# Performance work log

Hardware: AMD Instinct MI355X
Metric: run time of the kernel (lower is better)

Reference implementation:

```python
import jax, jax.numpy as jnp
import numpy as np

NP_, NT_, D_, E_, EP_, L_, R_ = 100000, 300000, 64, 2000000, 500000, 2, 2


def setup_inputs() -> dict:
    key = jax.random.key(0)
    ks = jax.random.split(key, 12)
    return {
        "emb_playlist": jax.random.normal(ks[0], (NP_, D_), jnp.float32),
        "emb_track": jax.random.normal(ks[1], (NT_, D_), jnp.float32),
        "W_rel": jax.random.normal(ks[2], (L_, R_, D_, D_), jnp.float32) * 0.1,
        "W_root": jax.random.normal(ks[3], (L_, D_, D_), jnp.float32) * 0.1,
        "bias": jnp.zeros((L_, D_), jnp.float32),
        "n_id_playlist": jnp.arange(NP_, dtype=jnp.int32),
        "n_id_track": jnp.arange(NT_, dtype=jnp.int32),
        "edge_pt_src": jax.random.randint(ks[4], (E_,), 0, NP_, jnp.int32),
        "edge_pt_dst": jax.random.randint(ks[5], (E_,), 0, NT_, jnp.int32),
        "edge_tp_src": jax.random.randint(ks[6], (E_,), 0, NT_, jnp.int32),
        "edge_tp_dst": jax.random.randint(ks[7], (E_,), 0, NP_, jnp.int32),
        "ell_pl": jax.random.randint(ks[8], (EP_,), 0, NP_, jnp.int32),
        "ell_tr": jax.random.randint(ks[9], (EP_,), 0, NT_, jnp.int32),
    }


def _hetero_gnn(emb_playlist, emb_track, W_rel, W_root, bias,
                n_id_playlist, n_id_track,
                edge_pt_src, edge_pt_dst, edge_tp_src, edge_tp_dst,
                ell_pl, ell_tr):
    NP = emb_playlist.shape[0]
    NT = emb_track.shape[0]
    L = W_root.shape[0]
    N = NP + NT

    # embedding lookup by n_id (identity here, but faithful gather)
    x_pl = emb_playlist[n_id_playlist]
    x_tr = emb_track[n_id_track]

    # alpha=None -> uniform 1/(L+1); buffer is softmaxed -> still uniform
    weights = jax.nn.softmax(jnp.full((L + 1,), 1.0 / (L + 1), jnp.float32))

    out_pl = x_pl * weights[0]
    out_tr = x_tr * weights[0]

    # homogeneous layout: playlists at [0, NP), tracks at [NP, NP+NT)
    x = jnp.concatenate([x_pl, x_tr], axis=0)
    rel_edges = [
        (edge_pt_src, edge_pt_dst + NP),   # playlist -> track
        (edge_tp_src + NP, edge_tp_dst),   # track -> playlist
    ]

    for i in range(L):
        # RGCNConv: root transform + per-relation mean aggregation
        h = x @ W_root[i] + bias[i]
        for r, (src, dst) in enumerate(rel_edges):
            hr = x @ W_rel[i, r]              # [N, D] transform-then-gather
            msg = hr[src]                     # [E, D]
            ssum = jax.ops.segment_sum(msg, dst, num_segments=N)
            cnt = jax.ops.segment_sum(jnp.ones_like(dst, dtype=x.dtype), dst,
                                      num_segments=N)
            h = h + ssum / jnp.maximum(cnt, 1.0)[:, None]
        x = jax.nn.relu(h)
        out_pl = out_pl + x[:NP] * weights[i + 1]
        out_tr = out_tr + x[NP:] * weights[i + 1]

    # global -> local mapping via searchsorted (faithful happy path)
    ps_idx = jnp.argsort(n_id_playlist)
    ps = n_id_playlist[ps_idx]
    pl_loc = ps_idx[jnp.clip(jnp.searchsorted(ps, ell_pl), 0, NP - 1)]
    ts_idx = jnp.argsort(n_id_track)
    ts = n_id_track[ts_idx]
    tr_loc = ts_idx[jnp.clip(jnp.searchsorted(ts, ell_tr), 0, NT - 1)]

    # dot-product link scores (dropout p=0.0 -> identity)
    return jnp.sum(out_pl[pl_loc] * out_tr[tr_loc], axis=-1)


def reference(emb_playlist, emb_track, W_rel, W_root, bias,
              n_id_playlist, n_id_track,
              edge_pt_src, edge_pt_dst, edge_tp_src, edge_tp_dst,
              ell_pl, ell_tr):
    return _hetero_gnn(emb_playlist, emb_track, W_rel, W_root, bias,
                       n_id_playlist, n_id_track,
                       edge_pt_src, edge_pt_dst, edge_tp_src, edge_tp_dst,
                       ell_pl, ell_tr)
```

## Files before the change

kernel.cpp:

```cpp
#include <hip/hip_runtime.h>
#include <stdint.h>

typedef __attribute__((ext_vector_type(8))) short bf16x8;
typedef __attribute__((ext_vector_type(4))) float f32x4;

#define BN 192

static __device__ __forceinline__ float b2f_lo(uint32_t w) {
  union { uint32_t u; float f; } c; c.u = w << 16; return c.f;
}
static __device__ __forceinline__ float b2f_hi(uint32_t w) {
  union { uint32_t u; float f; } c; c.u = w & 0xffff0000u; return c.f;
}
static __device__ __forceinline__ uint16_t f2b(float f) {
  union { float f; uint32_t u; } c; c.f = f;
  return (uint16_t)((c.u + 0x7fffu + ((c.u >> 16) & 1u)) >> 16);
}
static __device__ __forceinline__ f32x4 unpack4(uint2 t) {
  f32x4 r;
  r.x = b2f_lo(t.x); r.y = b2f_hi(t.x);
  r.z = b2f_lo(t.y); r.w = b2f_hi(t.y);
  return r;
}
static __device__ __forceinline__ void acc8(float* s, uint4 v) {
  s[0] += b2f_lo(v.x); s[1] += b2f_hi(v.x);
  s[2] += b2f_lo(v.y); s[3] += b2f_hi(v.y);
  s[4] += b2f_lo(v.z); s[5] += b2f_hi(v.z);
  s[6] += b2f_lo(v.w); s[7] += b2f_hi(v.w);
}

__global__ __launch_bounds__(256) void convert_kernel(
    const float* __restrict__ emb_pl, const float* __restrict__ emb_tr,
    uint16_t* __restrict__ xb, int NP, int N) {
  long g = (long)blockIdx.x * 256 + threadIdx.x;
  long base8 = g * 8;
  long total = (long)N * 64;
  if (base8 >= total) return;
  long plEnd = (long)NP * 64;
  const float* src = (base8 < plEnd) ? (emb_pl + base8) : (emb_tr + (base8 - plEnd));
  f32x4 a = *(const f32x4*)src;
  f32x4 b = *(const f32x4*)(src + 4);
  union { uint16_t h[8]; uint4 v; } o;
  o.h[0] = f2b(a.x); o.h[1] = f2b(a.y); o.h[2] = f2b(a.z); o.h[3] = f2b(a.w);
  o.h[4] = f2b(b.x); o.h[5] = f2b(b.y); o.h[6] = f2b(b.z); o.h[7] = f2b(b.w);
  *(uint4*)(xb + base8) = o.v;
}

__global__ __launch_bounds__(256) void bucket_hist_kernel(
    const int* __restrict__ pt_dst, const int* __restrict__ tp_dst,
    int* __restrict__ bucketCount, int E, int NP, int NB) {
  extern __shared__ int hist[];
  int t = threadIdx.x;
  for (int b = t; b < NB; b += 256) hist[b] = 0;
  __syncthreads();
  long total = 2L * E;
  long stride = (long)gridDim.x * 256;
  for (long e = (long)blockIdx.x * 256 + t; e < total; e += stride) {
    int dstG = (e < E) ? (NP + pt_dst[e]) : tp_dst[e - E];
    atomicAdd(&hist[dstG / BN], 1);
  }
  __syncthreads();
  for (int b = t; b < NB; b += 256) {
    int h = hist[b];
    if (h > 0) atomicAdd(&bucketCount[b], h);
  }
}

__global__ __launch_bounds__(1024) void bucket_scan_kernel(
    const int* __restrict__ bucketCount, int* __restrict__ bucketStart,
    int* __restrict__ gCursor, int NB) {
  __shared__ int s[1024];
  int t = threadIdx.x;
  int K = (NB + 1023) >> 10;
  int b0 = t * K;
  int local = 0;
  for (int j = 0; j < K; ++j) {
    int b = b0 + j;
    if (b < NB) local += bucketCount[b];
  }
  int acc = local;
  s[t] = local;
  __syncthreads();
  for (int off = 1; off < 1024; off <<= 1) {
    int u = (t >= off) ? s[t - off] : 0;
    __syncthreads();
    acc += u;
    s[t] = acc;
    __syncthreads();
  }
  int run = acc - local;
  for (int j = 0; j < K; ++j) {
    int b = b0 + j;
    if (b < NB) {
      bucketStart[b] = run;
      gCursor[b] = run;
      run += bucketCount[b];
    }
  }
}

__global__ __launch_bounds__(512) void partition_kernel(
    const int* __restrict__ pt_src, const int* __restrict__ pt_dst,
    const int* __restrict__ tp_src, const int* __restrict__ tp_dst,
    int* __restrict__ gCursor, uint32_t* __restrict__ pk,
    int E, int NP, int NB, int chunk) {
  extern __shared__ int lds[];
  int* hist = lds;
  int* base = lds + NB;
  int t = threadIdx.x;
  long e0 = (long)blockIdx.x * chunk;
  long e1 = e0 + chunk;
  long total = 2L * E;
  if (e1 > total) e1 = total;
  for (int b = t; b < NB; b += 512) hist[b] = 0;
  __syncthreads();
  for (long e = e0 + t; e < e1; e += 512) {
    int dstG = (e < E) ? (NP + pt_dst[e]) : tp_dst[e - E];
    atomicAdd(&hist[dstG / BN], 1);
  }
  __syncthreads();
  for (int b = t; b < NB; b += 512) {
    int h = hist[b];
    base[b] = (h > 0) ? atomicAdd(&gCursor[b], h) : 0;
    hist[b] = 0;
  }
  __syncthreads();
  for (long e = e0 + t; e < e1; e += 512) {
    int dstG, src;
    if (e < E) {
      dstG = NP + pt_dst[e];
      src = pt_src[e];
    } else {
      dstG = tp_dst[e - E];
      src = NP + tp_src[e - E];
    }
    int b = dstG / BN;
    int dl = dstG - b * BN;
    int pos = base[b] + atomicAdd(&hist[b], 1);
    pk[pos] = ((uint32_t)dl << 20) | (uint32_t)src;
  }
}

__global__ __launch_bounds__(256) void local_csr_kernel(
    const int* __restrict__ bucketStart, const int* __restrict__ bucketCount,
    const uint32_t* __restrict__ pk, int* __restrict__ rowptr,
    int* __restrict__ col, int N, int TEtotal) {
  __shared__ int hist[256];
  __shared__ int cur[256];
  int t = threadIdx.x;
  int b = blockIdx.x;
  hist[t] = 0;
  __syncthreads();
  int beg = bucketStart[b], num = bucketCount[b];
  for (int i = t; i < num; i += 256)
    atomicAdd(&hist[pk[beg + i] >> 20], 1);
  __syncthreads();
  int v = hist[t];
  int acc = v;
  cur[t] = v;
  __syncthreads();
  for (int off = 1; off < 256; off <<= 1) {
    int u = (t >= off) ? cur[t - off] : 0;
    __syncthreads();
    acc += u;
    cur[t] = acc;
    __syncthreads();
  }
  int excl = acc - v;
  int node = b * BN + t;
  if (t < BN && node < N) rowptr[node] = beg + excl;
  cur[t] = excl;
  __syncthreads();
  for (int i = t; i < num; i += 256) {
    uint32_t w = pk[beg + i];
    int dl = (int)(w >> 20);
    int pos = atomicAdd(&cur[dl], 1);
    col[beg + pos] = (int)(w & 0xFFFFFu);
  }
  if (b == 0 && t == 0) rowptr[N] = TEtotal;
}

__global__ __launch_bounds__(256) void pull_kernel(
    const int* __restrict__ rowptr, const int* __restrict__ col,
    const uint16_t* __restrict__ base, uint16_t* __restrict__ agg, int N) {
  int node = blockIdx.x * 32 + (threadIdx.x >> 3);
  int c = threadIdx.x & 7;
  if (node >= N) return;
  int beg = rowptr[node], end = rowptr[node + 1];
  float s[8] = {0, 0, 0, 0, 0, 0, 0, 0};
  const uint16_t* bp = base + c * 8;
  int i = beg;
  for (; i + 4 <= end; i += 4) {
    int c0 = col[i], c1 = col[i + 1], c2 = col[i + 2], c3 = col[i + 3];
    uint4 v0 = *(const uint4*)(bp + (size_t)c0 * 64);
    uint4 v1 = *(const uint4*)(bp + (size_t)c1 * 64);
    uint4 v2 = *(const uint4*)(bp + (size_t)c2 * 64);
    uint4 v3 = *(const uint4*)(bp + (size_t)c3 * 64);
    acc8(s, v0); acc8(s, v1); acc8(s, v2); acc8(s, v3);
  }
  for (; i < end; ++i)
    acc8(s, *(const uint4*)(bp + (size_t)col[i] * 64));
  int deg = end - beg;
  float inv = 1.0f / (float)(deg > 1 ? deg : 1);
  union { uint16_t h[8]; uint4 v; } o;
#pragma unroll
  for (int j = 0; j < 8; ++j) o.h[j] = f2b(s[j] * inv);
  *(uint4*)(agg + (size_t)node * 64 + c * 8) = o.v;
}

__global__ __launch_bounds__(256) void transform_kernel(
    const uint16_t* __restrict__ xpl, const uint16_t* __restrict__ xtr,
    const uint16_t* __restrict__ agg,
    const float* __restrict__ Wroot,
    const float* __restrict__ WrelP, const float* __restrict__ WrelT,
    const float* __restrict__ biasrow,
    uint16_t* __restrict__ xout, int NP, int NT, int BP) {
  int wave = threadIdx.x >> 6;
  int lane = threadIdx.x & 63;
  int m = lane & 15, q = lane >> 4;

  int wl, nw, ntiles, nodeBase;
  const uint16_t* xbase;
  const float* Wrel;
  if ((int)blockIdx.x < BP) {
    wl = blockIdx.x * 4 + wave; nw = BP * 4; ntiles = NP / 16;
    xbase = xpl; Wrel = WrelP; nodeBase = 0;
  } else {
    wl = (blockIdx.x - BP) * 4 + wave; nw = (gridDim.x - BP) * 4; ntiles = NT / 16;
    xbase = xtr; Wrel = WrelT; nodeBase = NP;
  }

  bf16x8 br[2][4], bl[2][4];
  for (int kc = 0; kc < 2; ++kc)
    for (int ct = 0; ct < 4; ++ct) {
      int n = 16 * ct + m;
      int k0 = 32 * kc + 8 * q;
      bf16x8 t0, t1;
      for (int i = 0; i < 8; ++i) {
        t0[i] = (short)f2b(Wroot[(size_t)(k0 + i) * 64 + n]);
        t1[i] = (short)f2b(Wrel[(size_t)(k0 + i) * 64 + n]);
      }
      br[kc][ct] = t0;
      bl[kc][ct] = t1;
    }
  float bv[4];
  for (int ct = 0; ct < 4; ++ct) bv[ct] = biasrow[16 * ct + m];

  for (int t = wl; t < ntiles; t += nw) {
    int rowLocal = t * 16 + m;
    int nodeG = nodeBase + rowLocal;
    const uint16_t* xrow = xbase + (size_t)rowLocal * 64;
    bf16x8 ax0 = *(const bf16x8*)(xrow + 8 * q);
    bf16x8 ax1 = *(const bf16x8*)(xrow + 32 + 8 * q);

    const uint16_t* arow = agg + (size_t)nodeG * 64;
    bf16x8 aa0 = *(const bf16x8*)(arow + 8 * q);
    bf16x8 aa1 = *(const bf16x8*)(arow + 32 + 8 * q);

    f32x4 acc[4];
#pragma unroll
    for (int ct = 0; ct < 4; ++ct) acc[ct] = (f32x4){bv[ct], bv[ct], bv[ct], bv[ct]};
#pragma unroll
    for (int ct = 0; ct < 4; ++ct) {
      acc[ct] = __builtin_amdgcn_mfma_f32_16x16x32_bf16(ax0, br[0][ct], acc[ct], 0, 0, 0);
      acc[ct] = __builtin_amdgcn_mfma_f32_16x16x32_bf16(ax1, br[1][ct], acc[ct], 0, 0, 0);
      acc[ct] = __builtin_amdgcn_mfma_f32_16x16x32_bf16(aa0, bl[0][ct], acc[ct], 0, 0, 0);
      acc[ct] = __builtin_amdgcn_mfma_f32_16x16x32_bf16(aa1, bl[1][ct], acc[ct], 0, 0, 0);
    }
    int nodeRow0 = nodeBase + t * 16;
#pragma unroll
    for (int ct = 0; ct < 4; ++ct)
#pragma unroll
      for (int r = 0; r < 4; ++r) {
        float v = acc[ct][r];
        v = v > 0.0f ? v : 0.0f;
        xout[(size_t)(nodeRow0 + 4 * q + r) * 64 + 16 * ct + m] = f2b(v);
      }
  }
}

__global__ __launch_bounds__(256) void sum_kernel(
    const float* __restrict__ emb_pl, const float* __restrict__ emb_tr,
    const uint16_t* __restrict__ x1, const uint16_t* __restrict__ x2,
    uint16_t* __restrict__ S, int NP, int N) {
  long g = (long)blockIdx.x * 256 + threadIdx.x;
  long b8 = g * 8;
  long total = (long)N * 64;
  if (b8 >= total) return;
  long plEnd = (long)NP * 64;
  const float* e = (b8 < plEnd) ? (emb_pl + b8) : (emb_tr + (b8 - plEnd));
  f32x4 ea = *(const f32x4*)e;
  f32x4 eb = *(const f32x4*)(e + 4);
  uint4 x1v = *(const uint4*)(x1 + b8);
  uint4 x2v = *(const uint4*)(x2 + b8);
  f32x4 fa1 = unpack4(make_uint2(x1v.x, x1v.y)), fb1 = unpack4(make_uint2(x1v.z, x1v.w));
  f32x4 fa2 = unpack4(make_uint2(x2v.x, x2v.y)), fb2 = unpack4(make_uint2(x2v.z, x2v.w));
  union { uint16_t h[8]; uint4 v; } o;
  o.h[0] = f2b(ea.x + fa1.x + fa2.x);
  o.h[1] = f2b(ea.y + fa1.y + fa2.y);
  o.h[2] = f2b(ea.z + fa1.z + fa2.z);
  o.h[3] = f2b(ea.w + fa1.w + fa2.w);
  o.h[4] = f2b(eb.x + fb1.x + fb2.x);
  o.h[5] = f2b(eb.y + fb1.y + fb2.y);
  o.h[6] = f2b(eb.z + fb1.z + fb2.z);
  o.h[7] = f2b(eb.w + fb1.w + fb2.w);
  *(uint4*)(S + b8) = o.v;
}

__global__ void score_kernel(const int* __restrict__ ell_pl,
                             const int* __restrict__ ell_tr,
                             const uint16_t* __restrict__ S,
                             float* __restrict__ out, int EP, int NP) {
  long g = (long)blockIdx.x * blockDim.x + threadIdx.x;
  long pair = g >> 3;
  int c = (int)(g & 7);
  if (pair >= EP) return;
  int p = ell_pl[pair];
  int t = ell_tr[pair];
  uint4 vp = *(const uint4*)(S + (size_t)p * 64 + c * 8);
  uint4 vt = *(const uint4*)(S + (size_t)(NP + t) * 64 + c * 8);
  float partial = b2f_lo(vp.x) * b2f_lo(vt.x) + b2f_hi(vp.x) * b2f_hi(vt.x)
                + b2f_lo(vp.y) * b2f_lo(vt.y) + b2f_hi(vp.y) * b2f_hi(vt.y)
                + b2f_lo(vp.z) * b2f_lo(vt.z) + b2f_hi(vp.z) * b2f_hi(vt.z)
                + b2f_lo(vp.w) * b2f_lo(vt.w) + b2f_hi(vp.w) * b2f_hi(vt.w);
  partial += __shfl_xor(partial, 1);
  partial += __shfl_xor(partial, 2);
  partial += __shfl_xor(partial, 4);
  if (c == 0) out[pair] = partial * (1.0f / 9.0f);
}

extern "C" void kernel_launch(void* const* d_in, const int* in_sizes, int n_in,
                              void* d_out, int out_size, void* d_ws, size_t ws_size,
                              hipStream_t stream) {
  const float* emb_pl = (const float*)d_in[0];
  const float* emb_tr = (const float*)d_in[1];
  const float* W_rel = (const float*)d_in[2];
  const float* W_root = (const float*)d_in[3];
  const float* bias = (const float*)d_in[4];
  const int* pt_src = (const int*)d_in[7];
  const int* pt_dst = (const int*)d_in[8];
  const int* tp_src = (const int*)d_in[9];
  const int* tp_dst = (const int*)d_in[10];
  const int* ell_pl = (const int*)d_in[11];
  const int* ell_tr = (const int*)d_in[12];
  float* out = (float*)d_out;

  const int NP = in_sizes[5];
  const int NT = in_sizes[6];
  const int E = in_sizes[7];
  const int EP = in_sizes[11];
  const int N = NP + NT;
  const long TE = 2L * E;
  const int NB = (N + BN - 1) / BN;

  char* ws = (char*)d_ws;
  size_t off = 0;
  uint16_t* agg = (uint16_t*)(ws + off); off += (size_t)N * 64 * 2;
  uint16_t* x1  = (uint16_t*)(ws + off); off += (size_t)N * 64 * 2;
  uint16_t* x2  = (uint16_t*)(ws + off); off += (size_t)N * 64 * 2;
  uint32_t* pk  = (uint32_t*)(ws + off); off += (size_t)TE * 4;
  int* col      = (int*)(ws + off);      off += (size_t)TE * 4;
  int* rowptr   = (int*)(ws + off);      off += (size_t)(N + 1) * 4;
  int* bucketCount = (int*)(ws + off);   off += (size_t)NB * 4;
  int* bucketStart = (int*)(ws + off);   off += (size_t)NB * 4;
  int* gCursor     = (int*)(ws + off);   off += (size_t)NB * 4;

  uint16_t* xb0 = x2;
  uint16_t* S = agg;

  const int TB = 256;
  const int PB = 256;
  int chunk = (int)((TE + PB - 1) / PB);
  long cvt = ((long)N * 64 / 8 + TB - 1) / TB;
  int pullBlocks = (N + 31) / 32;
  int scoreBlocks = (int)(((long)EP * 8 + TB - 1) / TB);
  const int BP = 256, GT = 1024;

  convert_kernel<<<(int)cvt, TB, 0, stream>>>(emb_pl, emb_tr, xb0, NP, N);

  hipMemsetAsync(bucketCount, 0, (size_t)NB * 4, stream);
  bucket_hist_kernel<<<128, TB, NB * 4, stream>>>(pt_dst, tp_dst, bucketCount,
                                                  E, NP, NB);
  bucket_scan_kernel<<<1, 1024, 0, stream>>>(bucketCount, bucketStart, gCursor, NB);
  partition_kernel<<<PB, 512, 2 * NB * 4, stream>>>(
      pt_src, pt_dst, tp_src, tp_dst, gCursor, pk, E, NP, NB, chunk);
  local_csr_kernel<<<NB, TB, 0, stream>>>(bucketStart, bucketCount, pk,
                                          rowptr, col, N, (int)TE);

  pull_kernel<<<pullBlocks, TB, 0, stream>>>(rowptr, col, xb0, agg, N);
  transform_kernel<<<GT, TB, 0, stream>>>(
      xb0, xb0 + (size_t)NP * 64, agg, W_root + 0 * 4096, W_rel + 1 * 4096,
      W_rel + 0 * 4096, bias + 0, x1, NP, NT, BP);

  pull_kernel<<<pullBlocks, TB, 0, stream>>>(rowptr, col, x1, agg, N);
  transform_kernel<<<GT, TB, 0, stream>>>(
      x1, x1 + (size_t)NP * 64, agg, W_root + 1 * 4096, W_rel + 3 * 4096,
      W_rel + 2 * 4096, bias + 64, x2, NP, NT, BP);

  sum_kernel<<<(int)cvt, TB, 0, stream>>>(emb_pl, emb_tr, x1, x2, S, NP, N);
  score_kernel<<<scoreBlocks, TB, 0, stream>>>(ell_pl, ell_tr, S, out, EP, NP);
}
```

Before: 596.0 us.

## Stage partitioned edges in LDS and widen CSR buckets to 1024 nodes

The partition kernel now processes fixed 8192-edge tiles and keeps each edge in registers. It computes a local per-bucket scan, then stages the (global position, packed edge) pairs in shared memory so they can be written out in bucket order. This is meant to turn scattered global stores into more clustered writes and to avoid re-reading the edge arrays. Buckets grow from 192 to 1024 nodes, shift replaces divide, and the local CSR kernel uses 512 threads with a two-per-thread scan. NB is capped at 512 (N=400000 gives 391), and the larger shared-memory footprint may limit occupancy.

```diff
diff --git a/kernel.cpp b/kernel.cpp
--- a/kernel.cpp
+++ b/kernel.cpp
@@ -4,7 +4,12 @@
 typedef __attribute__((ext_vector_type(8))) short bf16x8;
 typedef __attribute__((ext_vector_type(4))) float f32x4;
 
-#define BN 192
+#define BN 1024
+#define BNSHIFT 10
+#define MAXNB 512
+#define PTI 8192
+#define PTHREADS 512
+#define EPT (PTI / PTHREADS)
 
 static __device__ __forceinline__ float b2f_lo(uint32_t w) {
   union { uint32_t u; float f; } c; c.u = w << 16; return c.f;
@@ -57,7 +62,7 @@
   long stride = (long)gridDim.x * 256;
   for (long e = (long)blockIdx.x * 256 + t; e < total; e += stride) {
     int dstG = (e < E) ? (NP + pt_dst[e]) : tp_dst[e - E];
-    atomicAdd(&hist[dstG / BN], 1);
+    atomicAdd(&hist[dstG >> BNSHIFT], 1);
   }
   __syncthreads();
   for (int b = t; b < NB; b += 256) {
@@ -99,79 +104,124 @@
   }
 }
 
-__global__ __launch_bounds__(512) void partition_kernel(
+__global__ __launch_bounds__(PTHREADS) void partition_kernel(
     const int* __restrict__ pt_src, const int* __restrict__ pt_dst,
     const int* __restrict__ tp_src, const int* __restrict__ tp_dst,
     int* __restrict__ gCursor, uint32_t* __restrict__ pk,
-    int E, int NP, int NB, int chunk) {
-  extern __shared__ int lds[];
-  int* hist = lds;
-  int* base = lds + NB;
+    int E, int NP, int NB) {
+  __shared__ uint64_t buf[PTI];
+  __shared__ int hist[MAXNB];
+  __shared__ int lstart[MAXNB];
+  __shared__ int gbase[MAXNB];
+  __shared__ int cur[MAXNB];
+  __shared__ int sc[PTHREADS];
   int t = threadIdx.x;
-  long e0 = (long)blockIdx.x * chunk;
-  long e1 = e0 + chunk;
   long total = 2L * E;
-  if (e1 > total) e1 = total;
-  for (int b = t; b < NB; b += 512) hist[b] = 0;
-  __syncthreads();
-  for (long e = e0 + t; e < e1; e += 512) {
-    int dstG = (e < E) ? (NP + pt_dst[e]) : tp_dst[e - E];
-    atomicAdd(&hist[dstG / BN], 1);
-  }
-  __syncthreads();
-  for (int b = t; b < NB; b += 512) {
-    int h = hist[b];
-    base[b] = (h > 0) ? atomicAdd(&gCursor[b], h) : 0;
-    hist[b] = 0;
-  }
-  __syncthreads();
-  for (long e = e0 + t; e < e1; e += 512) {
-    int dstG, src;
-    if (e < E) {
-      dstG = NP + pt_dst[e];
-      src = pt_src[e];
-    } else {
-      dstG = tp_dst[e - E];
-      src = NP + tp_src[e - E];
+  long e0 = (long)blockIdx.x * PTI;
+  long rem = total - e0;
+  int cnt = (rem < (long)PTI) ? (int)rem : PTI;
+
+  for (int j = t; j < NB; j += PTHREADS) hist[j] = 0;
+  __syncthreads();
+
+  int bj[EPT];
+  uint32_t pkj[EPT];
+#pragma unroll
+  for (int j = 0; j < EPT; ++j) {
+    int i = j * PTHREADS + t;
+    bj[j] = -1;
+    if (i < cnt) {
+      long e = e0 + i;
+      int dstG, src;
+      if (e < E) {
+        dstG = NP + pt_dst[e];
+        src = pt_src[e];
+      } else {
+        dstG = tp_dst[e - E];
+        src = NP + tp_src[e - E];
+      }
+      int b = dstG >> BNSHIFT;
+      bj[j] = b;
+      pkj[j] = ((uint32_t)(dstG & (BN - 1)) << 20) | (uint32_t)src;
+      atomicAdd(&hist[b], 1);
     }
-    int b = dstG / BN;
-    int dl = dstG - b * BN;
-    int pos = base[b] + atomicAdd(&hist[b], 1);
-    pk[pos] = ((uint32_t)dl << 20) | (uint32_t)src;
-  }
-}
-
-__global__ __launch_bounds__(256) void local_csr_kernel(
+  }
+  __syncthreads();
+
+  int h = (t < NB) ? hist[t] : 0;
+  int acc = h;
+  sc[t] = h;
+  __syncthreads();
+  for (int off = 1; off < PTHREADS; off <<= 1) {
+    int u = (t >= off) ? sc[t - off] : 0;
+    __syncthreads();
+    acc += u;
+    sc[t] = acc;
+    __syncthreads();
+  }
+  if (t < NB) {
+    int ls = acc - h;
+    lstart[t] = ls;
+    cur[t] = ls;
+    gbase[t] = (h > 0) ? atomicAdd(&gCursor[t], h) : 0;
+  }
+  __syncthreads();
+
+#pragma unroll
+  for (int j = 0; j < EPT; ++j) {
+    int b = bj[j];
+    if (b >= 0) {
+      int pos = atomicAdd(&cur[b], 1);
+      int gpos = gbase[b] + (pos - lstart[b]);
+      buf[pos] = ((uint64_t)(uint32_t)gpos << 32) | (uint64_t)pkj[j];
+    }
+  }
+  __syncthreads();
+
+  for (int i = t; i < cnt; i += PTHREADS) {
+    uint64_t e = buf[i];
+    pk[(uint32_t)(e >> 32)] = (uint32_t)e;
+  }
+}
+
+__global__ __launch_bounds__(512) void local_csr_kernel(
     const int* __restrict__ bucketStart, const int* __restrict__ bucketCount,
     const uint32_t* __restrict__ pk, int* __restrict__ rowptr,
     int* __restrict__ col, int N, int TEtotal) {
-  __shared__ int hist[256];
-  __shared__ int cur[256];
+  __shared__ int hist[BN];
+  __shared__ int cur[BN];
+  __shared__ int ssum[512];
   int t = threadIdx.x;
   int b = blockIdx.x;
   hist[t] = 0;
+  hist[t + 512] = 0;
   __syncthreads();
   int beg = bucketStart[b], num = bucketCount[b];
-  for (int i = t; i < num; i += 256)
+  for (int i = t; i < num; i += 512)
     atomicAdd(&hist[pk[beg + i] >> 20], 1);
   __syncthreads();
-  int v = hist[t];
-  int acc = v;
-  cur[t] = v;
-  __syncthreads();
-  for (int off = 1; off < 256; off <<= 1) {
-    int u = (t >= off) ? cur[t - off] : 0;
+  int base0 = t * 2;
+  int h0 = hist[base0], h1 = hist[base0 + 1];
+  int tot = h0 + h1;
+  int acc = tot;
+  ssum[t] = tot;
+  __syncthreads();
+  for (int off = 1; off < 512; off <<= 1) {
+    int u = (t >= off) ? ssum[t - off] : 0;
     __syncthreads();
     acc += u;
-    cur[t] = acc;
-    __syncthreads();
-  }
-  int excl = acc - v;
-  int node = b * BN + t;
-  if (t < BN && node < N) rowptr[node] = beg + excl;
-  cur[t] = excl;
-  __syncthreads();
-  for (int i = t; i < num; i += 256) {
+    ssum[t] = acc;
+    __syncthreads();
+  }
+  int run = acc - tot;
+  int ex0 = run, ex1 = run + h0;
+  cur[base0] = ex0;
+  cur[base0 + 1] = ex1;
+  int node0 = (b << BNSHIFT) + base0;
+  if (node0 < N) rowptr[node0] = beg + ex0;
+  if (node0 + 1 < N) rowptr[node0 + 1] = beg + ex1;
+  __syncthreads();
+  for (int i = t; i < num; i += 512) {
     uint32_t w = pk[beg + i];
     int dl = (int)(w >> 20);
     int pos = atomicAdd(&cur[dl], 1);
@@ -369,11 +419,10 @@
   uint16_t* S = agg;
 
   const int TB = 256;
-  const int PB = 256;
-  int chunk = (int)((TE + PB - 1) / PB);
   long cvt = ((long)N * 64 / 8 + TB - 1) / TB;
   int pullBlocks = (N + 31) / 32;
   int scoreBlocks = (int)(((long)EP * 8 + TB - 1) / TB);
+  int partBlocks = (int)((TE + PTI - 1) / PTI);
   const int BP = 256, GT = 1024;
 
   convert_kernel<<<(int)cvt, TB, 0, stream>>>(emb_pl, emb_tr, xb0, NP, N);
@@ -382,10 +431,10 @@
   bucket_hist_kernel<<<128, TB, NB * 4, stream>>>(pt_dst, tp_dst, bucketCount,
                                                   E, NP, NB);
   bucket_scan_kernel<<<1, 1024, 0, stream>>>(bucketCount, bucketStart, gCursor, NB);
-  partition_kernel<<<PB, 512, 2 * NB * 4, stream>>>(
-      pt_src, pt_dst, tp_src, tp_dst, gCursor, pk, E, NP, NB, chunk);
-  local_csr_kernel<<<NB, TB, 0, stream>>>(bucketStart, bucketCount, pk,
-                                          rowptr, col, N, (int)TE);
+  partition_kernel<<<partBlocks, PTHREADS, 0, stream>>>(
+      pt_src, pt_dst, tp_src, tp_dst, gCursor, pk, E, NP, NB);
+  local_csr_kernel<<<NB, 512, 0, stream>>>(bucketStart, bucketCount, pk,
+                                           rowptr, col, N, (int)TE);
 
   pull_kernel<<<pullBlocks, TB, 0, stream>>>(rowptr, col, xb0, agg, N);
   transform_kernel<<<GT, TB, 0, stream>>>(
```

Result: faster. 554.1 us (-7.0%).
